# Optimization experiments

Measured on AMD Instinct MI355X. Metric: run time of the kernel, lower is better.

Reference implementation:

```python
import math
import jax, jax.numpy as jnp
import numpy as np

B, C_IN, H, W = 2, 64, 256, 512
C_OUT, KH, KW = 64, 3, 3
STRIDE, PAD, DIL = 1, 1, 1


def equi_offsets(pano_H, pano_W, kH, kW, dtype=jnp.float32):
    """Geometry-derived per-pixel offsets for equirectangular deform-conv.
    Returns (off_y, off_x), each [K, pano_H, pano_W], K = kH*kW (row-major)."""
    K = kH * kW
    u = jnp.arange(pano_W, dtype=dtype)
    v = jnp.arange(pano_H, dtype=dtype)
    phi = (u - pano_W / 2.0) / pano_W * (2.0 * math.pi)   # longitude per column
    theta = -(v - pano_H / 2.0) / pano_H * math.pi        # latitude per row
    # R_y(phi): [W,3,3]
    cp, sp = jnp.cos(phi), jnp.sin(phi)
    z, o = jnp.zeros_like(cp), jnp.ones_like(cp)
    Ry = jnp.stack([jnp.stack([cp, z, sp], -1),
                    jnp.stack([z, o, z], -1),
                    jnp.stack([-sp, z, cp], -1)], -2)
    # R_x(theta): [H,3,3]
    ct, st = jnp.cos(theta), jnp.sin(theta)
    zh, oh = jnp.zeros_like(ct), jnp.ones_like(ct)
    Rx = jnp.stack([jnp.stack([oh, zh, zh], -1),
                    jnp.stack([zh, ct, -st], -1),
                    jnp.stack([zh, st, ct], -1)], -2)
    ROT = jnp.einsum('wij,hjk->hwik', Ry, Rx)             # [H,W,3,3]
    # Pinhole rays for the kernel window
    fov_w = kW * (2.0 * math.pi / pano_W)
    focal = (kW / 2.0) / math.tan(fov_w / 2.0)
    hg = (jnp.arange(kH, dtype=dtype)[:, None] + 0.5 - kH / 2.0)
    wg = (jnp.arange(kW, dtype=dtype)[None, :] + 0.5 - kW / 2.0)
    hg = jnp.broadcast_to(hg, (kH, kW)).reshape(K)
    wg = jnp.broadcast_to(wg, (kH, kW)).reshape(K)
    rays0 = jnp.stack([wg / focal, hg / focal, jnp.ones(K, dtype)], 0)  # inv_K @ [w,h,1]
    rays0 = rays0 / jnp.linalg.norm(rays0, axis=0, keepdims=True)
    rays = jnp.einsum('hwik,kn->hwin', ROT, rays0)        # [H,W,3,K]
    phi2 = jnp.arctan2(rays[..., 0, :], rays[..., 2, :])
    th2 = jnp.arcsin(jnp.clip(rays[..., 1, :], -1.0, 1.0))
    x = pano_W / (2.0 * math.pi) * phi2 + pano_W / 2.0    # [H,W,K]
    y = pano_H / math.pi * th2 + pano_H / 2.0
    off_x = x - (wg[None, None, :] + u[None, :, None])
    off_y = y - (hg[None, None, :] + v[:, None, None])
    return jnp.transpose(off_y, (2, 0, 1)), jnp.transpose(off_x, (2, 0, 1))


def deform_conv2d(x, weight, bias, off_y, off_x, stride, pad, dil):
    """Deformable conv (groups=1) with zero-padded bilinear sampling.
    x: [B,C,Hi,Wi]; weight: [O,C,kH,kW]; off_y/off_x: [K,Ho,Wo]."""
    Bn, C, Hi, Wi = x.shape
    O, _, kH, kW = weight.shape
    K, Ho, Wo = off_y.shape
    ky = jnp.broadcast_to(jnp.arange(kH)[:, None], (kH, kW)).reshape(K).astype(x.dtype)
    kx = jnp.broadcast_to(jnp.arange(kW)[None, :], (kH, kW)).reshape(K).astype(x.dtype)
    base_y = jnp.arange(Ho, dtype=x.dtype) * stride - pad
    base_x = jnp.arange(Wo, dtype=x.dtype) * stride - pad
    py = base_y[None, :, None] + ky[:, None, None] * dil + off_y   # [K,Ho,Wo]
    px = base_x[None, None, :] + kx[:, None, None] * dil + off_x
    y0f = jnp.floor(py)
    x0f = jnp.floor(px)
    wy1 = py - y0f
    wx1 = px - x0f
    iy0 = y0f.astype(jnp.int32)
    ix0 = x0f.astype(jnp.int32)
    iy1, ix1 = iy0 + 1, ix0 + 1
    xf = x.reshape(Bn, C, Hi * Wi)

    def corner(iy, ix, w):
        valid = (iy >= 0) & (iy < Hi) & (ix >= 0) & (ix < Wi)
        idx = jnp.clip(iy, 0, Hi - 1) * Wi + jnp.clip(ix, 0, Wi - 1)
        g = xf[:, :, idx]                                  # [B,C,K,Ho,Wo]
        return g * (w * valid.astype(x.dtype))[None, None]

    samp = (corner(iy0, ix0, (1 - wy1) * (1 - wx1))
            + corner(iy0, ix1, (1 - wy1) * wx1)
            + corner(iy1, ix0, wy1 * (1 - wx1))
            + corner(iy1, ix1, wy1 * wx1))                 # [B,C,K,Ho,Wo]
    out = jnp.einsum('bckhw,ock->bohw', samp, weight.reshape(O, C, K))
    return out + bias[None, :, None, None]


def setup_inputs() -> dict:
    key = jax.random.key(0)
    k1, k2, k3 = jax.random.split(key, 3)
    x = jax.random.normal(k1, (B, C_IN, H, W), dtype=jnp.float32)
    fan_in = C_IN * KH * KW
    weight = jax.random.normal(k2, (C_OUT, C_IN, KH, KW), dtype=jnp.float32) / math.sqrt(fan_in)
    bias = jax.random.normal(k3, (C_OUT,), dtype=jnp.float32) * 0.01
    return {"x": x, "weight": weight, "bias": bias}


def reference(x, weight, bias):
    Hi, Wi = x.shape[-2:]
    pano_W = (Wi + 2 * PAD - DIL * (KW - 1) - 1) // STRIDE + 1
    pano_H = (Hi + 2 * PAD - DIL * (KH - 1) - 1) // STRIDE + 1
    off_y, off_x = equi_offsets(pano_H, pano_W, KH, KW, x.dtype)
    return deform_conv2d(x, weight, bias, off_y, off_x, STRIDE, PAD, DIL)
```

## Files before the change

### kernel.cpp

```cpp
#include <hip/hip_runtime.h>
#include <math.h>

namespace {

typedef short  short8 __attribute__((ext_vector_type(8)));
typedef float  f32x4  __attribute__((ext_vector_type(4)));

constexpr int BB = 2, CC = 64, HH = 256, WW = 512, OO = 64, KK = 9;
constexpr int PXB  = 128;
constexpr int NGRP = 32;
constexpr int CHW_F = 6 * WW;
constexpr int BUF_F = 2 * CHW_F;
constexpr int SSTR  = 42;

__device__ __forceinline__ uint rne_bf16(float f) {
  uint u = __float_as_uint(f);
  return (u + 0x7fffu + ((u >> 16) & 1u)) >> 16;
}

__global__ __launch_bounds__(256, 2) void equiconv_mfma(
    const float* __restrict__ x, const float* __restrict__ wgt,
    const float* __restrict__ bias, float* __restrict__ out)
{
  __shared__ __align__(16) float  lbx[2][BUF_F];
  __shared__ __align__(16) ushort Sb[PXB * SSTR];

  const int tid  = threadIdx.x;
  const int wid  = tid >> 6, lane = tid & 63;
  const int p    = wid * 32 + (lane & 31);
  const int cc   = lane >> 5;
  const int w    = blockIdx.x * PXB + p;
  const int h    = blockIdx.y;
  const int b    = blockIdx.z;

  int   jx[KK][4];
  float cw[KK][4];
  {
#pragma clang fp contract(off)
    const float TWO_PI_F = (float)(2.0 * M_PI);
    const float PI_F     = (float)M_PI;
    const float XS       = (float)(512.0 / (2.0 * M_PI));
    const float YS       = (float)(256.0 / M_PI);

    const float uf = (float)w, vf = (float)h;
    const float phi   = ((uf - 256.0f) / 512.0f) * TWO_PI_F;
    const float theta = ((-(vf - 128.0f)) / 256.0f) * PI_F;

    const float sp = (float)sin((double)phi);
    const float cp = (float)cos((double)phi);
    const float st = (float)sin((double)theta);
    const float ct = (float)cos((double)theta);

    const float R00 = cp;        const float R01 = sp * st;  const float R02 = sp * ct;
                    const float R11 = ct;       const float R12 = -st;
    const float R20 = -sp;       const float R21 = cp * st;  const float R22 = cp * ct;

    const double focal_d = 1.5 / tan(0.5 * (3.0 * (2.0 * M_PI / 512.0)));
    const float  focal_f = (float)focal_d;

    for (int k = 0; k < KK; ++k) {
      const float wgk = (float)(k % 3) + 0.5f - 1.5f;
      const float hgk = (float)(k / 3) + 0.5f - 1.5f;

      float rx0 = wgk / focal_f, ry0 = hgk / focal_f, rz0 = 1.0f;
      const float nrm = sqrtf(((rx0 * rx0) + (ry0 * ry0)) + (rz0 * rz0));
      rx0 = rx0 / nrm; ry0 = ry0 / nrm; rz0 = rz0 / nrm;

      const float r0 = ((R00 * rx0) + (R01 * ry0)) + (R02 * rz0);
      const float r1 =               ((R11 * ry0)) + (R12 * rz0);
      const float r2 = ((R20 * rx0) + (R21 * ry0)) + (R22 * rz0);

      const float phi2 = (float)atan2((double)r0, (double)r2);
      float r1c = r1;
      if (r1c >  1.0f) r1c =  1.0f;
      if (r1c < -1.0f) r1c = -1.0f;
      const float th2 = (float)asin((double)r1c);

      const float xx = (XS * phi2) + 256.0f;
      const float yy = (YS * th2)  + 128.0f;

      const float Ax = (float)(w + (k % 3) - 1);
      const float Ay = (float)(h + (k / 3) - 1);
      const float px = Ax + (xx - Ax);
      const float py = Ay + (yy - Ay);

      const float x0f = floorf(px), y0f = floorf(py);
      const float wx1 = px - x0f,   wy1 = py - y0f;
      const int ix0 = (int)x0f, iy0 = (int)y0f;
      const int ix1 = ix0 + 1,  iy1 = iy0 + 1;
      const bool vx0 = (ix0 >= 0) && (ix0 < WW);
      const bool vx1 = (ix1 >= 0) && (ix1 < WW);
      const bool vy0 = (iy0 >= 0) && (iy0 < HH);
      const bool vy1 = (iy1 >= 0) && (iy1 < HH);
      const int cx0 = min(max(ix0, 0), WW - 1);
      const int cx1 = min(max(ix1, 0), WW - 1);
      const int cy0 = min(max(iy0, 0), HH - 1);
      const int cy1 = min(max(iy1, 0), HH - 1);
      const int j0 = cy0 - h + 2;
      const int j1 = cy1 - h + 2;
      jx[k][0] = j0 * WW + cx0;
      jx[k][1] = j0 * WW + cx1;
      jx[k][2] = j1 * WW + cx0;
      jx[k][3] = j1 * WW + cx1;
      const float wy0f = 1.0f - wy1, wx0f = 1.0f - wx1;
      cw[k][0] = (wy0f * wx0f) * ((vy0 && vx0) ? 1.0f : 0.0f);
      cw[k][1] = (wy0f * wx1)  * ((vy0 && vx1) ? 1.0f : 0.0f);
      cw[k][2] = (wy1 * wx0f)  * ((vy1 && vx0) ? 1.0f : 0.0f);
      cw[k][3] = (wy1 * wx1)   * ((vy1 && vx1) ? 1.0f : 0.0f);
    }
  }

  {
    uint* S32 = (uint*)Sb;
#pragma unroll
    for (int i = 0; i < 11; ++i) {
      const int idx = tid + 256 * i;
      if (idx < (PXB * SSTR) / 2) S32[idx] = 0u;
    }
  }

  auto stage = [&](int bi, int g2) {
#pragma unroll
    for (int i = 0; i < 6; ++i) {
      const int ci  = wid * 6 + i;
      const int ccs = ci / 12, r2 = ci % 12, j = r2 >> 1, half = r2 & 1;
      const int srow = min(max(h - 2 + j, 0), HH - 1);
      const int ch   = g2 * 2 + ccs;
      const float* src = x + (((size_t)b * CC + ch) * HH + srow) * WW + half * 256 + lane * 4;
      __builtin_amdgcn_global_load_lds(
          (const __attribute__((address_space(1))) void*)src,
          (__attribute__((address_space(3))) void*)&lbx[bi][ccs * CHW_F + j * 512 + half * 256],
          16, 0, 0);
    }
  };

  f32x4 acc[4][2];
#pragma unroll
  for (int ot = 0; ot < 4; ++ot)
#pragma unroll
    for (int pt = 0; pt < 2; ++pt) acc[ot][pt] = (f32x4){0.f, 0.f, 0.f, 0.f};

  stage(0, 0);

#pragma unroll 1
  for (int g = 0; g < NGRP; ++g) {
    const int bi = g & 1;

    short8 A[4];
    {
      const int lg = lane >> 4;
      const int c  = g * 2 + (lg >> 1);
#pragma unroll
      for (int ot = 0; ot < 4; ++ot) {
        const int o = ot * 16 + (lane & 15);
        const float* wp9 = wgt + ((size_t)o * 64 + c) * 9;
        short8 a;
        if ((lg & 1) == 0) {
#pragma unroll
          for (int j = 0; j < 8; ++j) a[j] = (short)(ushort)rne_bf16(wp9[j]);
        } else {
          a = (short8){0, 0, 0, 0, 0, 0, 0, 0};
          a[0] = (short)(ushort)rne_bf16(wp9[8]);
        }
        A[ot] = a;
      }
    }
    __builtin_amdgcn_sched_barrier(0);

    if (g < NGRP - 1) {
      stage(bi ^ 1, g + 1);
      asm volatile("s_waitcnt vmcnt(6)" ::: "memory");
    } else {
      asm volatile("s_waitcnt vmcnt(0)" ::: "memory");
    }
    __builtin_amdgcn_sched_barrier(0);
    __builtin_amdgcn_s_barrier();
    __builtin_amdgcn_sched_barrier(0);

    {
      const float* Lc = &lbx[bi][cc * CHW_F];
      float s[KK];
#pragma unroll
      for (int k = 0; k < KK; ++k) {
        s[k] = fmaf(cw[k][3], Lc[jx[k][3]],
               fmaf(cw[k][2], Lc[jx[k][2]],
               fmaf(cw[k][1], Lc[jx[k][1]],
                    cw[k][0] * Lc[jx[k][0]])));
      }
      const uint b0 = rne_bf16(s[0]), b1 = rne_bf16(s[1]), b2 = rne_bf16(s[2]);
      const uint b3 = rne_bf16(s[3]), b4 = rne_bf16(s[4]), b5 = rne_bf16(s[5]);
      const uint b6 = rne_bf16(s[6]), b7 = rne_bf16(s[7]), b8 = rne_bf16(s[8]);
      uint2* Sr = (uint2*)(Sb + p * SSTR + cc * 16);
      Sr[0] = make_uint2(b0 | (b1 << 16), b2 | (b3 << 16));
      Sr[1] = make_uint2(b4 | (b5 << 16), b6 | (b7 << 16));
      Sb[p * SSTR + cc * 16 + 8] = (ushort)b8;
    }

    asm volatile("s_waitcnt lgkmcnt(0)" ::: "memory");
    __builtin_amdgcn_sched_barrier(0);

    short8 Bfr[2];
#pragma unroll
    for (int pt = 0; pt < 2; ++pt) {
      const int prow = wid * 32 + pt * 16 + (lane & 15);
      Bfr[pt] = *(const short8*)(Sb + prow * SSTR + ((lane >> 4) & 3) * 8);
    }
    asm volatile("s_waitcnt lgkmcnt(0)" ::: "memory");
    __builtin_amdgcn_sched_barrier(0);
#pragma unroll
    for (int ot = 0; ot < 4; ++ot)
#pragma unroll
      for (int pt = 0; pt < 2; ++pt)
        acc[ot][pt] = __builtin_amdgcn_mfma_f32_16x16x32_bf16(A[ot], Bfr[pt], acc[ot][pt], 0, 0, 0);
    __builtin_amdgcn_sched_barrier(0);
  }

#pragma unroll
  for (int ot = 0; ot < 4; ++ot) {
    const int o = ot * 16 + ((lane >> 4) & 3) * 4;
#pragma unroll
    for (int pt = 0; pt < 2; ++pt) {
      const int wcol = blockIdx.x * PXB + wid * 32 + pt * 16 + (lane & 15);
#pragma unroll
      for (int r = 0; r < 4; ++r)
        out[(((size_t)b * OO + (o + r)) * HH + h) * WW + wcol] = acc[ot][pt][r] + bias[o + r];
    }
  }
}

}

extern "C" void kernel_launch(void* const* d_in, const int* in_sizes, int n_in,
                              void* d_out, int out_size, void* d_ws, size_t ws_size,
                              hipStream_t stream) {
  const float* x      = (const float*)d_in[0];
  const float* weight = (const float*)d_in[1];
  const float* bias   = (const float*)d_in[2];
  float* out          = (float*)d_out;

  dim3 grid(WW / PXB, HH, BB);
  hipLaunchKernelGGL(equiconv_mfma, grid, dim3(256), 0, stream,
                     x, weight, bias, out);
}
```

Measured before the change: 372.3 us.

## Triple-buffer input rows, prefetch weights, trim staged rows, swizzle block order

Moves from a double-buffered to a triple-buffered LDS pipeline, so input staging runs two groups ahead and the weight fragments for the next group are loaded into registers during the MFMA phase. It stages 5 rows per channel instead of 6, which cuts LDS footprint and global traffic. It also remaps the block index with a swizzle so concurrently scheduled blocks cover different rows or batches, which changes cache locality. The costs are more LDS per block and more live registers, both of which could lower occupancy, and the vmcnt bookkeeping is harder to get right.

```diff
diff --git a/kernel.cpp b/kernel.cpp
--- a/kernel.cpp
+++ b/kernel.cpp
@@ -9,7 +9,7 @@
 constexpr int BB = 2, CC = 64, HH = 256, WW = 512, OO = 64, KK = 9;
 constexpr int PXB  = 128;
 constexpr int NGRP = 32;
-constexpr int CHW_F = 6 * WW;
+constexpr int CHW_F = 5 * WW;
 constexpr int BUF_F = 2 * CHW_F;
 constexpr int SSTR  = 42;
 
@@ -22,16 +22,20 @@
     const float* __restrict__ x, const float* __restrict__ wgt,
     const float* __restrict__ bias, float* __restrict__ out)
 {
-  __shared__ __align__(16) float  lbx[2][BUF_F];
+  __shared__ __align__(16) float  lbx[3][BUF_F];
   __shared__ __align__(16) ushort Sb[PXB * SSTR];
+
+  const int id  = blockIdx.x + 4 * blockIdx.y + 1024 * blockIdx.z;
+  const int swz = (id & 7) * 256 + (id >> 3);
+  const int bx  = swz & 3;
+  const int h   = (swz >> 2) & 255;
+  const int b   = swz >> 10;
 
   const int tid  = threadIdx.x;
   const int wid  = tid >> 6, lane = tid & 63;
   const int p    = wid * 32 + (lane & 31);
   const int cc   = lane >> 5;
-  const int w    = blockIdx.x * PXB + p;
-  const int h    = blockIdx.y;
-  const int b    = blockIdx.z;
+  const int w    = bx * PXB + p;
 
   int   jx[KK][4];
   float cw[KK][4];
@@ -117,13 +121,14 @@
       const int idx = tid + 256 * i;
       if (idx < (PXB * SSTR) / 2) S32[idx] = 0u;
     }
+    asm volatile("s_waitcnt lgkmcnt(0)" ::: "memory");
   }
 
   auto stage = [&](int bi, int g2) {
 #pragma unroll
-    for (int i = 0; i < 6; ++i) {
-      const int ci  = wid * 6 + i;
-      const int ccs = ci / 12, r2 = ci % 12, j = r2 >> 1, half = r2 & 1;
+    for (int i = 0; i < 5; ++i) {
+      const int ci  = wid * 5 + i;
+      const int ccs = ci / 10, r2 = ci % 10, j = r2 >> 1, half = r2 & 1;
       const int srow = min(max(h - 2 + j, 0), HH - 1);
       const int ch   = g2 * 2 + ccs;
       const float* src = x + (((size_t)b * CC + ch) * HH + srow) * WW + half * 256 + lane * 4;
@@ -134,6 +139,22 @@
     }
   };
 
+  float araw[4][8];
+  auto loadA = [&](int g2) {
+    const int lg = lane >> 4;
+    const int c  = g2 * 2 + (lg >> 1);
+#pragma unroll
+    for (int ot = 0; ot < 4; ++ot) {
+      const float* wp9 = wgt + ((size_t)(ot * 16 + (lane & 15)) * 64 + c) * 9;
+      if ((lg & 1) == 0) {
+#pragma unroll
+        for (int j = 0; j < 8; ++j) araw[ot][j] = wp9[j];
+      } else {
+        araw[ot][0] = wp9[8];
+      }
+    }
+  };
+
   f32x4 acc[4][2];
 #pragma unroll
   for (int ot = 0; ot < 4; ++ot)
@@ -141,41 +162,38 @@
     for (int pt = 0; pt < 2; ++pt) acc[ot][pt] = (f32x4){0.f, 0.f, 0.f, 0.f};
 
   stage(0, 0);
+  __builtin_amdgcn_sched_barrier(0);
+  loadA(0);
+  __builtin_amdgcn_sched_barrier(0);
+  stage(1, 1);
+  __builtin_amdgcn_sched_barrier(0);
 
 #pragma unroll 1
   for (int g = 0; g < NGRP; ++g) {
-    const int bi = g & 1;
+    const int bi = g % 3;
+
+    if (g < NGRP - 1) { asm volatile("s_waitcnt vmcnt(5)" ::: "memory"); }
+    else              { asm volatile("s_waitcnt vmcnt(0)" ::: "memory"); }
+    __builtin_amdgcn_sched_barrier(0);
+    __builtin_amdgcn_s_barrier();
+    __builtin_amdgcn_sched_barrier(0);
 
     short8 A[4];
     {
       const int lg = lane >> 4;
-      const int c  = g * 2 + (lg >> 1);
 #pragma unroll
       for (int ot = 0; ot < 4; ++ot) {
-        const int o = ot * 16 + (lane & 15);
-        const float* wp9 = wgt + ((size_t)o * 64 + c) * 9;
         short8 a;
         if ((lg & 1) == 0) {
 #pragma unroll
-          for (int j = 0; j < 8; ++j) a[j] = (short)(ushort)rne_bf16(wp9[j]);
+          for (int j = 0; j < 8; ++j) a[j] = (short)(ushort)rne_bf16(araw[ot][j]);
         } else {
           a = (short8){0, 0, 0, 0, 0, 0, 0, 0};
-          a[0] = (short)(ushort)rne_bf16(wp9[8]);
+          a[0] = (short)(ushort)rne_bf16(araw[ot][0]);
         }
         A[ot] = a;
       }
     }
-    __builtin_amdgcn_sched_barrier(0);
-
-    if (g < NGRP - 1) {
-      stage(bi ^ 1, g + 1);
-      asm volatile("s_waitcnt vmcnt(6)" ::: "memory");
-    } else {
-      asm volatile("s_waitcnt vmcnt(0)" ::: "memory");
-    }
-    __builtin_amdgcn_sched_barrier(0);
-    __builtin_amdgcn_s_barrier();
-    __builtin_amdgcn_sched_barrier(0);
 
     {
       const float* Lc = &lbx[bi][cc * CHW_F];
@@ -213,6 +231,9 @@
       for (int pt = 0; pt < 2; ++pt)
         acc[ot][pt] = __builtin_amdgcn_mfma_f32_16x16x32_bf16(A[ot], Bfr[pt], acc[ot][pt], 0, 0, 0);
     __builtin_amdgcn_sched_barrier(0);
+
+    if (g + 1 < NGRP) { loadA(g + 1); __builtin_amdgcn_sched_barrier(0); }
+    if (g + 2 < NGRP) { stage((g + 2) % 3, g + 2); __builtin_amdgcn_sched_barrier(0); }
   }
 
 #pragma unroll
@@ -220,7 +241,7 @@
     const int o = ot * 16 + ((lane >> 4) & 3) * 4;
 #pragma unroll
     for (int pt = 0; pt < 2; ++pt) {
-      const int wcol = blockIdx.x * PXB + wid * 32 + pt * 16 + (lane & 15);
+      const int wcol = bx * PXB + wid * 32 + pt * 16 + (lane & 15);
 #pragma unroll
       for (int r = 0; r < 4; ++r)
         out[(((size_t)b * OO + (o + r)) * HH + h) * WW + wcol] = acc[ot][pt][r] + bias[o + r];
```

After: 500.3 us. +34.4%, slower.
